# Kernel tuning notes

Hardware: AMD Instinct MI355X
Metric: run time of the kernel (lower is better)

Reference implementation:

```python
import jax, jax.numpy as jnp
import numpy as np


def _gcn(G, A, x, W, b):
    # G: (K,N,N) chebyshev supports, A: (B,N,N) attention, x: (B,N,p)
    s = jnp.einsum('kij,bjp->bkip', G, x)          # graph conv per cheb order
    s = jnp.einsum('bij,bkjp->bikp', A, s)         # attention bmm, -> (B,N,K,p)
    B, N, K, p = s.shape
    s = s.reshape(B, N, K * p)                     # concat over k (k-major blocks)
    return s @ W + b


def setup_inputs() -> dict:
    key = jax.random.key(0)
    ks = jax.random.split(key, 8)
    B, T, N, C = 16, 12, 1024, 1
    K, H = 3, 64
    din = C + H  # 65
    x = jax.random.normal(ks[0], (B, T, N, C), dtype=jnp.float32)
    G = jax.random.normal(ks[1], (K, N, N), dtype=jnp.float32) / np.sqrt(N)
    A = jax.random.uniform(ks[2], (B, N, N), dtype=jnp.float32) / N
    W_gate = jax.random.normal(ks[3], (K * din, 2 * H), dtype=jnp.float32) * 0.02
    b_gate = jnp.zeros((2 * H,), dtype=jnp.float32)
    W_update = jax.random.normal(ks[4], (K * din, H), dtype=jnp.float32) * 0.02
    b_update = jnp.zeros((H,), dtype=jnp.float32)
    W_dec = jax.random.normal(ks[5], (H, 12 * 1), dtype=jnp.float32) * 0.02
    b_dec = jnp.zeros((12,), dtype=jnp.float32)
    return {"x": x, "G": G, "A": A, "W_gate": W_gate, "b_gate": b_gate,
            "W_update": W_update, "b_update": b_update, "W_dec": W_dec, "b_dec": b_dec}


def reference(x, G, A, W_gate, b_gate, W_update, b_update, W_dec, b_dec):
    B, T, N, _ = x.shape
    H = W_update.shape[1]
    out_steps, output_dim = 12, 1

    def step(h, xt):
        combined = jnp.concatenate([xt, h], axis=-1)              # (B,N,din)
        zr = jax.nn.sigmoid(_gcn(G, A, combined, W_gate, b_gate))  # (B,N,2H)
        z, r = zr[..., :H], zr[..., H:]
        cand = jnp.concatenate([xt, r * h], axis=-1)
        hc = jnp.tanh(_gcn(G, A, cand, W_update, b_update))
        h_new = z * hc + (1.0 - z) * h
        return h_new, None

    h0 = jnp.zeros((B, N, H), dtype=x.dtype)
    h_last, _ = jax.lax.scan(step, h0, jnp.swapaxes(x, 0, 1))      # scan over T
    out = h_last @ W_dec + b_dec                                   # (B,N,out_steps*output_dim)
    out = out.reshape(B, N, out_steps, output_dim)
    return jnp.transpose(out, (0, 2, 1, 3))                        # (B,out_steps,N,output_dim)
```

## Files before the change

kernel.cpp:

```cpp
#include <hip/hip_runtime.h>

#define B_  16
#define T_  12
#define N_  1024
#define K_  3
#define H_  64
#define DIN 65
#define KH  192
#define OG  128

typedef _Float16 f16x4 __attribute__((ext_vector_type(4)));
typedef _Float16 f16x8 __attribute__((ext_vector_type(8)));
typedef float    f32x4 __attribute__((ext_vector_type(4)));

static const size_t OFF_H   = 0;
static const size_t OFF_ZB  = 1048576;
static const size_t OFF_S2  = 2097152;
static const size_t OFF_HTA = 2686976;
static const size_t OFF_HTB = 3211264;
static const size_t OFF_S1  = 3735552;
static const size_t OFF_WGT = 4030464;
static const size_t OFF_WUT = 4042752;
static const size_t OFF_WX  = 4048896;
static const size_t OFF_GT  = 4049472;
static const size_t OFF_AG  = 5622336;

__global__ __launch_bounds__(256) void k_repack(const float* __restrict__ Wg,
                                                const float* __restrict__ Wu,
                                                _Float16* __restrict__ wghT,
                                                _Float16* __restrict__ wuhT,
                                                float* __restrict__ wx) {
    const float inv = 1.0f / 1024.0f;
    int idx = blockIdx.x * 256 + threadIdx.x;
    if (idx < 128 * 192) {
        int o = idx / 192, d = idx % 192;
        int k = d / 64, c = d % 64;
        wghT[idx] = (_Float16)(Wg[(size_t)(k * DIN + 1 + c) * OG + o] * inv);
    } else if (idx < 128 * 192 + 64 * 192) {
        int j = idx - 128 * 192;
        int o = j / 192, d = j % 192;
        int k = d / 64, c = d % 64;
        wuhT[j] = (_Float16)(Wu[(size_t)(k * DIN + 1 + c) * H_ + o] * inv);
    } else if (idx < 128 * 192 + 64 * 192 + 576) {
        int j = idx - 128 * 192 - 64 * 192;
        if (j < 384) { int k = j >> 7, o = j & 127; wx[j] = Wg[(size_t)(k * DIN) * OG + o] * inv; }
        else { int j2 = j - 384; int k = j2 >> 6, o = j2 & 63; wx[j] = Wu[(size_t)(k * DIN) * H_ + o] * inv; }
    }
}

__global__ __launch_bounds__(256) void k_gtr(const float* __restrict__ G,
                                             _Float16* __restrict__ GfT) {
    int bx = blockIdx.x;
    int kk = bx >> 8, rem = bx & 255, ti = rem >> 4, tj = rem & 15;
    int i0 = ti * 64, j0 = tj * 64;
    __shared__ _Float16 s[64][72];
    int tid = threadIdx.x;
    int r = tid >> 2, cb = (tid & 3) * 16;
    const float* Gp = G + ((size_t)kk << 20) + ((size_t)(i0 + r) << 10) + j0 + cb;
    #pragma unroll
    for (int q = 0; q < 4; ++q) {
        float4 v = *(const float4*)&Gp[q * 4];
        f16x4 hv = {(_Float16)v.x, (_Float16)v.y, (_Float16)v.z, (_Float16)v.w};
        *(f16x4*)&s[r][cb + q * 4] = hv;
    }
    __syncthreads();
    alignas(16) _Float16 tmp[16];
    #pragma unroll
    for (int q = 0; q < 16; ++q) tmp[q] = s[cb + q][r];
    _Float16* outp = GfT + ((size_t)kk << 20) + ((size_t)(j0 + r) << 10) + i0 + cb;
    *(f16x8*)&outp[0] = *(f16x8*)&tmp[0];
    *(f16x8*)&outp[8] = *(f16x8*)&tmp[8];
}

__global__ __launch_bounds__(256) void k_ag(const float* __restrict__ A,
                                            const _Float16* __restrict__ GfT,
                                            _Float16* __restrict__ AG) {
    int bx = blockIdx.x;
    int inst = bx >> 6, tile = bx & 63;
    int b = inst / 3, kk = inst % 3;
    int i0 = (tile >> 3) * 128, j0 = (tile & 7) * 128;
    __shared__ _Float16 sA[2][128][72], sB[2][128][72];
    int tid = threadIdx.x;
    int w = tid >> 6, lane = tid & 63, ln = lane & 15, kg = lane >> 4;
    int mq = (w & 1) * 64, nq = (w >> 1) * 64;
    int srow = tid >> 1, cb = (tid & 1) * 32;
    const float*    qa = A   + ((size_t)b << 20)  + ((size_t)(i0 + srow) << 10) + cb;
    const _Float16* qb = GfT + ((size_t)kk << 20) + ((size_t)(j0 + srow) << 10) + cb;

    f32x4 acc[4][4];
    #pragma unroll
    for (int mt = 0; mt < 4; ++mt)
        #pragma unroll
        for (int nt = 0; nt < 4; ++nt) acc[mt][nt] = (f32x4){0.f, 0.f, 0.f, 0.f};

    float4 ra[8]; f16x8 rb[4];
    #pragma unroll
    for (int q = 0; q < 8; ++q) ra[q] = *(const float4*)&qa[q * 4];
    #pragma unroll
    for (int q = 0; q < 4; ++q) rb[q] = *(const f16x8*)&qb[q * 8];
    #pragma unroll
    for (int q = 0; q < 4; ++q) {
        float4 u = ra[2*q], v = ra[2*q+1];
        f16x8 hv = {(_Float16)(u.x*1024.f), (_Float16)(u.y*1024.f), (_Float16)(u.z*1024.f), (_Float16)(u.w*1024.f),
                    (_Float16)(v.x*1024.f), (_Float16)(v.y*1024.f), (_Float16)(v.z*1024.f), (_Float16)(v.w*1024.f)};
        *(f16x8*)&sA[0][srow][cb + q * 8] = hv;
        *(f16x8*)&sB[0][srow][cb + q * 8] = rb[q];
    }
    __syncthreads();

    for (int tt = 0; tt < 16; ++tt) {
        int cur = tt & 1;
        if (tt < 15) {
            int kn = (tt + 1) * 64;
            #pragma unroll
            for (int q = 0; q < 8; ++q) ra[q] = *(const float4*)&qa[kn + q * 4];
            #pragma unroll
            for (int q = 0; q < 4; ++q) rb[q] = *(const f16x8*)&qb[kn + q * 8];
        }
        #pragma unroll
        for (int ks = 0; ks < 2; ++ks) {
            int ko = ks * 32 + kg * 8;
            f16x8 a[4], bfr[4];
            #pragma unroll
            for (int mt = 0; mt < 4; ++mt) a[mt] = *(const f16x8*)&sA[cur][mq + mt * 16 + ln][ko];
            #pragma unroll
            for (int nt = 0; nt < 4; ++nt) bfr[nt] = *(const f16x8*)&sB[cur][nq + nt * 16 + ln][ko];
            #pragma unroll
            for (int mt = 0; mt < 4; ++mt)
                #pragma unroll
                for (int nt = 0; nt < 4; ++nt)
                    acc[mt][nt] = __builtin_amdgcn_mfma_f32_16x16x32_f16(a[mt], bfr[nt], acc[mt][nt], 0, 0, 0);
        }
        if (tt < 15) {
            int nb = cur ^ 1;
            #pragma unroll
            for (int q = 0; q < 4; ++q) {
                float4 u = ra[2*q], v = ra[2*q+1];
                f16x8 hv = {(_Float16)(u.x*1024.f), (_Float16)(u.y*1024.f), (_Float16)(u.z*1024.f), (_Float16)(u.w*1024.f),
                            (_Float16)(v.x*1024.f), (_Float16)(v.y*1024.f), (_Float16)(v.z*1024.f), (_Float16)(v.w*1024.f)};
                *(f16x8*)&sA[nb][srow][cb + q * 8] = hv;
                *(f16x8*)&sB[nb][srow][cb + q * 8] = rb[q];
            }
            __syncthreads();
        }
    }

    _Float16* outp = AG + ((size_t)(b * 3 + kk) << 20);
    #pragma unroll
    for (int mt = 0; mt < 4; ++mt)
        #pragma unroll
        for (int r = 0; r < 4; ++r) {
            int i = i0 + mq + mt * 16 + kg * 4 + r;
            #pragma unroll
            for (int nt = 0; nt < 4; ++nt) {
                int j = j0 + nq + nt * 16 + ln;
                outp[((size_t)i << 10) + j] = (_Float16)acc[mt][nt][r];
            }
        }
}

__global__ __launch_bounds__(256) void k_s1b(const float* __restrict__ G,
                                             const float* __restrict__ x,
                                             _Float16* __restrict__ S1) {
    int bx = blockIdx.x;
    int nh = bx & 1, it = (bx >> 1) & 15, kk = bx >> 5;
    int i0 = it * 64, m0 = nh * 96;
    __shared__ _Float16 sA[64][72], sB[96][72];
    int tid = threadIdx.x, wid = tid >> 6, ln = tid & 15, kl = (tid & 63) >> 4;
    const float* Gk = G + (size_t)kk * N_ * N_;
    f32x4 acc[6];
    #pragma unroll
    for (int n = 0; n < 6; ++n) acc[n] = (f32x4){0.f, 0.f, 0.f, 0.f};
    for (int kc = 0; kc < N_; kc += 64) {
        #pragma unroll
        for (int it2 = 0; it2 < 4; ++it2) {
            int idx = it2 * 256 + tid; int row = idx >> 4, c4 = (idx & 15) * 4;
            float4 g = *(const float4*)&Gk[(size_t)(i0 + row) * N_ + kc + c4];
            f16x4 hv = {(_Float16)g.x, (_Float16)g.y, (_Float16)g.z, (_Float16)g.w};
            *(f16x4*)&sA[row][c4] = hv;
        }
        #pragma unroll
        for (int it2 = 0; it2 < 6; ++it2) {
            int idx = it2 * 256 + tid; int row = idx >> 4, c4 = (idx & 15) * 4;
            float4 g = *(const float4*)&x[(size_t)(m0 + row) * N_ + kc + c4];
            f16x4 hv = {(_Float16)g.x, (_Float16)g.y, (_Float16)g.z, (_Float16)g.w};
            *(f16x4*)&sB[row][c4] = hv;
        }
        __syncthreads();
        #pragma unroll
        for (int ks = 0; ks < 4; ++ks) {
            int ko = ks * 16 + kl * 4;
            f16x4 a = *(const f16x4*)&sA[wid * 16 + ln][ko];
            #pragma unroll
            for (int n = 0; n < 6; ++n) {
                f16x4 b = *(const f16x4*)&sB[n * 16 + ln][ko];
                acc[n] = __builtin_amdgcn_mfma_f32_16x16x16f16(a, b, acc[n], 0, 0, 0);
            }
        }
        __syncthreads();
    }
    #pragma unroll
    for (int n = 0; n < 6; ++n) {
        int m = m0 + n * 16 + ln;
        #pragma unroll
        for (int r = 0; r < 4; ++r) {
            int i = i0 + wid * 16 + kl * 4 + r;
            S1[(((size_t)kk * 192 + m) << 10) + i] = (_Float16)acc[n][r];
        }
    }
}

__global__ __launch_bounds__(256) void k_s2b(const float* __restrict__ A,
                                             const _Float16* __restrict__ S1,
                                             float* __restrict__ S2) {
    int bx = blockIdx.x; int it = bx & 15, b = bx >> 4; int i0 = it * 64;
    __shared__ _Float16 sA[64][72], sB[48][72];
    int tid = threadIdx.x, wid = tid >> 6, ln = tid & 15, kl = (tid & 63) >> 4;
    const float* Ab = A + (size_t)b * N_ * N_;
    f32x4 acc[3];
    #pragma unroll
    for (int n = 0; n < 3; ++n) acc[n] = (f32x4){0.f, 0.f, 0.f, 0.f};
    for (int kc = 0; kc < N_; kc += 64) {
        #pragma unroll
        for (int it2 = 0; it2 < 4; ++it2) {
            int idx = it2 * 256 + tid; int row = idx >> 4, c4 = (idx & 15) * 4;
            float4 a4 = *(const float4*)&Ab[(size_t)(i0 + row) * N_ + kc + c4];
            f16x4 hv = {(_Float16)(a4.x * 1024.f), (_Float16)(a4.y * 1024.f),
                        (_Float16)(a4.z * 1024.f), (_Float16)(a4.w * 1024.f)};
            *(f16x4*)&sA[row][c4] = hv;
        }
        for (int idx = tid; idx < 288; idx += 256) {
            int row = idx >> 3, c8 = (idx & 7) * 8;
            int kq = row / 12, tq = row - kq * 12;
            *(uint4*)&sB[row][c8] = *(const uint4*)&S1[(((size_t)kq * 192 + b * T_ + tq) << 10) + kc + c8];
        }
        __syncthreads();
        #pragma unroll
        for (int ks = 0; ks < 4; ++ks) {
            int ko = ks * 16 + kl * 4;
            f16x4 a = *(const f16x4*)&sA[wid * 16 + ln][ko];
            #pragma unroll
            for (int n = 0; n < 3; ++n) {
                f16x4 b = *(const f16x4*)&sB[n * 16 + ln][ko];
                acc[n] = __builtin_amdgcn_mfma_f32_16x16x16f16(a, b, acc[n], 0, 0, 0);
            }
        }
        __syncthreads();
    }
    #pragma unroll
    for (int n = 0; n < 3; ++n) {
        int col = n * 16 + ln;
        if (col < 36) {
            int kq = col / 12, tq = col - kq * 12;
            #pragma unroll
            for (int r = 0; r < 4; ++r) {
                int i = i0 + wid * 16 + kl * 4 + r;
                S2[(((size_t)(b * 3 + kq) * T_ + tq) << 10) + i] = acc[n][r];
            }
        }
    }
}

__global__ __launch_bounds__(256) void k_fzr(const _Float16* __restrict__ AG,
                                             const _Float16* __restrict__ HtIn,
                                             const _Float16* __restrict__ wghT,
                                             const float* __restrict__ wx,
                                             const float* __restrict__ bg,
                                             const float* __restrict__ S2,
                                             const float* __restrict__ h,
                                             float* __restrict__ zb,
                                             _Float16* __restrict__ HtOut, int t) {
    int bx = blockIdx.x; int it = bx & 31, b = bx >> 5; int i0 = it * 32;
    __shared__ __align__(16) char smem[46080];
    _Float16 (*sA)[96][72] = reinterpret_cast<_Float16(*)[96][72]>(smem);
    _Float16 (*sB)[64][72] = reinterpret_cast<_Float16(*)[64][72]>(smem + 27648);
    _Float16 (*sZ)[200]    = reinterpret_cast<_Float16(*)[200]>(smem);
    _Float16 (*sW)[72]     = reinterpret_cast<_Float16(*)[72]>(smem + 12800);
    __shared__ float sS2[3][32];
    __shared__ float sWX[384];
    __shared__ float sBias[128];
    int tid = threadIdx.x;
    int w = tid >> 6, lane = tid & 63, ln = lane & 15, kg = lane >> 4;
    if (tid < 96) { int k = tid >> 5, il = tid & 31; sS2[k][il] = S2[(((size_t)(b * 3 + k) * T_ + t) << 10) + i0 + il]; }
    for (int q = tid; q < 384; q += 256) sWX[q] = wx[q];
    if (tid < 128) sBias[tid] = bg[tid];

    int srow = tid >> 3, sc8 = (tid & 7) * 8;
    const _Float16* pa0 = AG + ((size_t)(b * 3 + 0) << 20) + ((size_t)(i0 + srow) << 10) + sc8;
    const _Float16* pa1 = AG + ((size_t)(b * 3 + 1) << 20) + ((size_t)(i0 + srow) << 10) + sc8;
    const _Float16* pa2 = AG + ((size_t)(b * 3 + 2) << 20) + ((size_t)(i0 + srow) << 10) + sc8;
    const _Float16* pb0 = HtIn + ((size_t)b << 16) + ((size_t)srow << 10) + sc8;
    const _Float16* pb1 = HtIn + ((size_t)b << 16) + ((size_t)(srow + 32) << 10) + sc8;

    f32x4 acc[2][3];
    #pragma unroll
    for (int m = 0; m < 2; ++m)
        #pragma unroll
        for (int n = 0; n < 3; ++n) acc[m][n] = (f32x4){0.f, 0.f, 0.f, 0.f};

    f16x8 rA0 = *(const f16x8*)pa0, rA1 = *(const f16x8*)pa1, rA2 = *(const f16x8*)pa2;
    f16x8 rB0 = *(const f16x8*)pb0, rB1 = *(const f16x8*)pb1;
    *(f16x8*)&sA[0][srow][sc8] = rA0;
    *(f16x8*)&sA[0][32 + srow][sc8] = rA1;
    *(f16x8*)&sA[0][64 + srow][sc8] = rA2;
    *(f16x8*)&sB[0][srow][sc8] = rB0;
    *(f16x8*)&sB[0][srow + 32][sc8] = rB1;
    __syncthreads();

    int kbF = (w * 3) >> 2, kbL = (w * 3 + 2) >> 2;
    for (int tt = 0; tt < 16; ++tt) {
        int cur = tt & 1;
        if (tt < 15) {
            int kn = (tt + 1) * 64;
            rA0 = *(const f16x8*)&pa0[kn]; rA1 = *(const f16x8*)&pa1[kn]; rA2 = *(const f16x8*)&pa2[kn];
            rB0 = *(const f16x8*)&pb0[kn]; rB1 = *(const f16x8*)&pb1[kn];
        }
        #pragma unroll
        for (int ks = 0; ks < 2; ++ks) {
            int ko = ks * 32 + kg * 8;
            f16x8 aF0 = *(const f16x8*)&sA[cur][kbF * 32 + ln][ko];
            f16x8 aF1 = *(const f16x8*)&sA[cur][kbF * 32 + 16 + ln][ko];
            f16x8 aL0 = *(const f16x8*)&sA[cur][kbL * 32 + ln][ko];
            f16x8 aL1 = *(const f16x8*)&sA[cur][kbL * 32 + 16 + ln][ko];
            #pragma unroll
            for (int ni = 0; ni < 3; ++ni) {
                int ct = w * 3 + ni;
                f16x8 bb = *(const f16x8*)&sB[cur][(ct & 3) * 16 + ln][ko];
                bool late = (ct >> 2) != kbF;
                f16x8 a0 = late ? aL0 : aF0;
                f16x8 a1 = late ? aL1 : aF1;
                acc[0][ni] = __builtin_amdgcn_mfma_f32_16x16x32_f16(a0, bb, acc[0][ni], 0, 0, 0);
                acc[1][ni] = __builtin_amdgcn_mfma_f32_16x16x32_f16(a1, bb, acc[1][ni], 0, 0, 0);
            }
        }
        if (tt < 15) {
            int nb = cur ^ 1;
            *(f16x8*)&sA[nb][srow][sc8] = rA0;
            *(f16x8*)&sA[nb][32 + srow][sc8] = rA1;
            *(f16x8*)&sA[nb][64 + srow][sc8] = rA2;
            *(f16x8*)&sB[nb][srow][sc8] = rB0;
            *(f16x8*)&sB[nb][srow + 32][sc8] = rB1;
            __syncthreads();
        }
    }
    __syncthreads();

    #pragma unroll
    for (int m = 0; m < 2; ++m)
        #pragma unroll
        for (int ni = 0; ni < 3; ++ni)
            #pragma unroll
            for (int r = 0; r < 4; ++r)
                sZ[m * 16 + kg * 4 + r][(w * 3 + ni) * 16 + ln] = (_Float16)acc[m][ni][r];

    f32x4 e[2][2];
    #pragma unroll
    for (int m = 0; m < 2; ++m)
        #pragma unroll
        for (int n = 0; n < 2; ++n) e[m][n] = (f32x4){0.f, 0.f, 0.f, 0.f};
    for (int kc = 0; kc < 192; kc += 64) {
        #pragma unroll
        for (int it2 = 0; it2 < 4; ++it2) {
            int idx = it2 * 256 + tid; int row = idx >> 3, c8 = (idx & 7) * 8;
            *(f16x8*)&sW[row][c8] = *(const f16x8*)&wghT[(size_t)row * 192 + kc + c8];
        }
        __syncthreads();
        #pragma unroll
        for (int ks = 0; ks < 4; ++ks) {
            int ko = ks * 16 + kg * 4;
            f16x4 az0 = *(const f16x4*)&sZ[ln][kc + ko];
            f16x4 az1 = *(const f16x4*)&sZ[16 + ln][kc + ko];
            f16x4 bw0 = *(const f16x4*)&sW[w * 32 + ln][ko];
            f16x4 bw1 = *(const f16x4*)&sW[w * 32 + 16 + ln][ko];
            e[0][0] = __builtin_amdgcn_mfma_f32_16x16x16f16(az0, bw0, e[0][0], 0, 0, 0);
            e[0][1] = __builtin_amdgcn_mfma_f32_16x16x16f16(az0, bw1, e[0][1], 0, 0, 0);
            e[1][0] = __builtin_amdgcn_mfma_f32_16x16x16f16(az1, bw0, e[1][0], 0, 0, 0);
            e[1][1] = __builtin_amdgcn_mfma_f32_16x16x16f16(az1, bw1, e[1][1], 0, 0, 0);
        }
        __syncthreads();
    }

    #pragma unroll
    for (int n = 0; n < 2; ++n) {
        int o = w * 32 + n * 16 + ln;
        float w0 = sWX[o], w1 = sWX[128 + o], w2 = sWX[256 + o], bi = sBias[o];
        if (o < H_) {
            #pragma unroll
            for (int m = 0; m < 2; ++m)
                #pragma unroll
                for (int r = 0; r < 4; ++r) {
                    int il = m * 16 + kg * 4 + r;
                    float pre = e[m][n][r] + w0 * sS2[0][il] + w1 * sS2[1][il] + w2 * sS2[2][il] + bi;
                    float v = 1.0f / (1.0f + expf(-pre));
                    zb[((size_t)((b << 10) + i0 + il)) * H_ + o] = v;
                }
        } else {
            int c = o - H_;
            #pragma unroll
            for (int m = 0; m < 2; ++m) {
                alignas(8) _Float16 hb[4];
                #pragma unroll
                for (int r = 0; r < 4; ++r) {
                    int il = m * 16 + kg * 4 + r;
                    float pre = e[m][n][r] + w0 * sS2[0][il] + w1 * sS2[1][il] + w2 * sS2[2][il] + bi;
                    float v = 1.0f / (1.0f + expf(-pre));
                    hb[r] = (_Float16)(v * h[((size_t)((b << 10) + i0 + il)) * H_ + c]);
                }
                *(f16x4*)&HtOut[((size_t)(b * 64 + c) << 10) + i0 + m * 16 + kg * 4] = *(f16x4*)&hb[0];
            }
        }
    }
}

__global__ __launch_bounds__(256) void k_fup(const _Float16* __restrict__ AG,
                                             const _Float16* __restrict__ HtIn,
                                             const _Float16* __restrict__ wuhT,
                                             const float* __restrict__ wx,
                                             const float* __restrict__ bu,
                                             const float* __restrict__ S2,
                                             const float* __restrict__ zb,
                                             float* __restrict__ h,
                                             _Float16* __restrict__ HtOut, int t) {
    int bx = blockIdx.x; int it = bx & 31, b = bx >> 5; int i0 = it * 32;
    __shared__ __align__(16) char smem[46080];
    _Float16 (*sA)[96][72] = reinterpret_cast<_Float16(*)[96][72]>(smem);
    _Float16 (*sB)[64][72] = reinterpret_cast<_Float16(*)[64][72]>(smem + 27648);
    _Float16 (*sZ)[200]    = reinterpret_cast<_Float16(*)[200]>(smem);
    _Float16 (*sW)[72]     = reinterpret_cast<_Float16(*)[72]>(smem + 12800);
    __shared__ float sS2[3][32];
    __shared__ float sWX[192];
    __shared__ float sBias[64];
    int tid = threadIdx.x;
    int w = tid >> 6, lane = tid & 63, ln = lane & 15, kg = lane >> 4;
    if (tid < 96) { int k = tid >> 5, il = tid & 31; sS2[k][il] = S2[(((size_t)(b * 3 + k) * T_ + t) << 10) + i0 + il]; }
    if (tid < 192) sWX[tid] = wx[384 + tid];
    if (tid < 64) sBias[tid] = bu[tid];

    int srow = tid >> 3, sc8 = (tid & 7) * 8;
    const _Float16* pa0 = AG + ((size_t)(b * 3 + 0) << 20) + ((size_t)(i0 + srow) << 10) + sc8;
    const _Float16* pa1 = AG + ((size_t)(b * 3 + 1) << 20) + ((size_t)(i0 + srow) << 10) + sc8;
    const _Float16* pa2 = AG + ((size_t)(b * 3 + 2) << 20) + ((size_t)(i0 + srow) << 10) + sc8;
    const _Float16* pb0 = HtIn + ((size_t)b << 16) + ((size_t)srow << 10) + sc8;
    const _Float16* pb1 = HtIn + ((size_t)b << 16) + ((size_t)(srow + 32) << 10) + sc8;

    f32x4 acc[2][3];
    #pragma unroll
    for (int m = 0; m < 2; ++m)
        #pragma unroll
        for (int n = 0; n < 3; ++n) acc[m][n] = (f32x4){0.f, 0.f, 0.f, 0.f};

    f16x8 rA0 = *(const f16x8*)pa0, rA1 = *(const f16x8*)pa1, rA2 = *(const f16x8*)pa2;
    f16x8 rB0 = *(const f16x8*)pb0, rB1 = *(const f16x8*)pb1;
    *(f16x8*)&sA[0][srow][sc8] = rA0;
    *(f16x8*)&sA[0][32 + srow][sc8] = rA1;
    *(f16x8*)&sA[0][64 + srow][sc8] = rA2;
    *(f16x8*)&sB[0][srow][sc8] = rB0;
    *(f16x8*)&sB[0][srow + 32][sc8] = rB1;
    __syncthreads();

    int kbF = (w * 3) >> 2, kbL = (w * 3 + 2) >> 2;
    for (int tt = 0; tt < 16; ++tt) {
        int cur = tt & 1;
        if (tt < 15) {
            int kn = (tt + 1) * 64;
            rA0 = *(const f16x8*)&pa0[kn]; rA1 = *(const f16x8*)&pa1[kn]; rA2 = *(const f16x8*)&pa2[kn];
            rB0 = *(const f16x8*)&pb0[kn]; rB1 = *(const f16x8*)&pb1[kn];
        }
        #pragma unroll
        for (int ks = 0; ks < 2; ++ks) {
            int ko = ks * 32 + kg * 8;
            f16x8 aF0 = *(const f16x8*)&sA[cur][kbF * 32 + ln][ko];
            f16x8 aF1 = *(const f16x8*)&sA[cur][kbF * 32 + 16 + ln][ko];
            f16x8 aL0 = *(const f16x8*)&sA[cur][kbL * 32 + ln][ko];
            f16x8 aL1 = *(const f16x8*)&sA[cur][kbL * 32 + 16 + ln][ko];
            #pragma unroll
            for (int ni = 0; ni < 3; ++ni) {
                int ct = w * 3 + ni;
                f16x8 bb = *(const f16x8*)&sB[cur][(ct & 3) * 16 + ln][ko];
                bool late = (ct >> 2) != kbF;
                f16x8 a0 = late ? aL0 : aF0;
                f16x8 a1 = late ? aL1 : aF1;
                acc[0][ni] = __builtin_amdgcn_mfma_f32_16x16x32_f16(a0, bb, acc[0][ni], 0, 0, 0);
                acc[1][ni] = __builtin_amdgcn_mfma_f32_16x16x32_f16(a1, bb, acc[1][ni], 0, 0, 0);
            }
        }
        if (tt < 15) {
            int nb = cur ^ 1;
            *(f16x8*)&sA[nb][srow][sc8] = rA0;
            *(f16x8*)&sA[nb][32 + srow][sc8] = rA1;
            *(f16x8*)&sA[nb][64 + srow][sc8] = rA2;
            *(f16x8*)&sB[nb][srow][sc8] = rB0;
            *(f16x8*)&sB[nb][srow + 32][sc8] = rB1;
            __syncthreads();
        }
    }
    __syncthreads();

    #pragma unroll
    for (int m = 0; m < 2; ++m)
        #pragma unroll
        for (int ni = 0; ni < 3; ++ni)
            #pragma unroll
            for (int r = 0; r < 4; ++r)
                sZ[m * 16 + kg * 4 + r][(w * 3 + ni) * 16 + ln] = (_Float16)acc[m][ni][r];

    f32x4 e[2];
    e[0] = (f32x4){0.f, 0.f, 0.f, 0.f};
    e[1] = (f32x4){0.f, 0.f, 0.f, 0.f};
    for (int kc = 0; kc < 192; kc += 64) {
        #pragma unroll
        for (int it2 = 0; it2 < 2; ++it2) {
            int idx = it2 * 256 + tid; int row = idx >> 3, c8 = (idx & 7) * 8;
            *(f16x8*)&sW[row][c8] = *(const f16x8*)&wuhT[(size_t)row * 192 + kc + c8];
        }
        __syncthreads();
        #pragma unroll
        for (int ks = 0; ks < 4; ++ks) {
            int ko = ks * 16 + kg * 4;
            f16x4 az0 = *(const f16x4*)&sZ[ln][kc + ko];
            f16x4 az1 = *(const f16x4*)&sZ[16 + ln][kc + ko];
            f16x4 bw  = *(const f16x4*)&sW[w * 16 + ln][ko];
            e[0] = __builtin_amdgcn_mfma_f32_16x16x16f16(az0, bw, e[0], 0, 0, 0);
            e[1] = __builtin_amdgcn_mfma_f32_16x16x16f16(az1, bw, e[1], 0, 0, 0);
        }
        __syncthreads();
    }

    int o = w * 16 + ln;
    float w0 = sWX[o], w1 = sWX[64 + o], w2 = sWX[128 + o], bi = sBias[o];
    #pragma unroll
    for (int m = 0; m < 2; ++m) {
        alignas(8) _Float16 hb[4];
        #pragma unroll
        for (int r = 0; r < 4; ++r) {
            int il = m * 16 + kg * 4 + r;
            float pre = e[m][r] + w0 * sS2[0][il] + w1 * sS2[1][il] + w2 * sS2[2][il] + bi;
            float hc = tanhf(pre);
            size_t gi = ((size_t)((b << 10) + i0 + il)) * H_ + o;
            float z = zb[gi], hold = h[gi];
            float hn = z * hc + (1.0f - z) * hold;
            h[gi] = hn;
            hb[r] = (_Float16)hn;
        }
        *(f16x4*)&HtOut[((size_t)(b * 64 + o) << 10) + i0 + m * 16 + kg * 4] = *(f16x4*)&hb[0];
    }
}

__global__ __launch_bounds__(256) void k_dec(const float* __restrict__ h,
                                             const float* __restrict__ Wd,
                                             const float* __restrict__ bd,
                                             float* __restrict__ out) {
    int bx = blockIdx.x;
    int b = bx >> 4, it = bx & 15; int i0 = it * 64;
    __shared__ float hs[64][65];
    __shared__ float Wds[64][12];
    __shared__ float bds[12];
    int tid = threadIdx.x;
    for (int idx = tid; idx < 4096; idx += 256) {
        int r = idx >> 6, c = idx & 63;
        hs[r][c] = h[(size_t)(b * N_ + i0 + r) * H_ + c];
    }
    for (int idx = tid; idx < 768; idx += 256)
        Wds[idx / 12][idx % 12] = Wd[idx];
    if (tid < 12) bds[tid] = bd[tid];
    __syncthreads();
    for (int oidx = tid; oidx < 768; oidx += 256) {
        int i = oidx & 63, tt = oidx >> 6;
        float acc = bds[tt];
        #pragma unroll
        for (int c = 0; c < 64; ++c) acc += hs[i][c] * Wds[c][tt];
        out[(size_t)(b * T_ + tt) * N_ + i0 + i] = acc;
    }
}

extern "C" void kernel_launch(void* const* d_in, const int* in_sizes, int n_in,
                              void* d_out, int out_size, void* d_ws, size_t ws_size,
                              hipStream_t stream) {
    const float* x  = (const float*)d_in[0];
    const float* G  = (const float*)d_in[1];
    const float* A  = (const float*)d_in[2];
    const float* Wg = (const float*)d_in[3];
    const float* bg = (const float*)d_in[4];
    const float* Wu = (const float*)d_in[5];
    const float* bu = (const float*)d_in[6];
    const float* Wd = (const float*)d_in[7];
    const float* bd = (const float*)d_in[8];
    float* out = (float*)d_out;
    float* ws  = (float*)d_ws;

    float* h   = ws + OFF_H;
    float* zb  = ws + OFF_ZB;
    float* S2  = ws + OFF_S2;
    float* wxb = ws + OFF_WX;
    _Float16* HtA  = (_Float16*)(ws + OFF_HTA);
    _Float16* HtB  = (_Float16*)(ws + OFF_HTB);
    _Float16* S1   = (_Float16*)(ws + OFF_S1);
    _Float16* wghT = (_Float16*)(ws + OFF_WGT);
    _Float16* wuhT = (_Float16*)(ws + OFF_WUT);
    _Float16* GfT  = (_Float16*)(ws + OFF_GT);
    _Float16* AG   = (_Float16*)(ws + OFF_AG);

    hipMemsetAsync(h, 0, (size_t)B_ * N_ * H_ * sizeof(float), stream);
    hipMemsetAsync((void*)HtA, 0, (size_t)B_ * N_ * H_ * sizeof(_Float16), stream);
    k_repack<<<147, 256, 0, stream>>>(Wg, Wu, wghT, wuhT, wxb);
    k_gtr<<<768, 256, 0, stream>>>(G, GfT);
    k_ag<<<3072, 256, 0, stream>>>(A, GfT, AG);
    k_s1b<<<96, 256, 0, stream>>>(G, x, S1);
    k_s2b<<<256, 256, 0, stream>>>(A, S1, S2);

    for (int t = 0; t < T_; ++t) {
        k_fzr<<<512, 256, 0, stream>>>(AG, HtA, wghT, wxb, bg, S2, h, zb, HtB, t);
        k_fup<<<512, 256, 0, stream>>>(AG, HtB, wuhT, wxb, bu, S2, zb, h, HtA, t);
    }
    k_dec<<<256, 256, 0, stream>>>(h, Wd, bd, out);
}
```

Baseline: 960.7 us.

## Pre-convert A to fp16 once, swizzle AG block order, halve recurrent row tiles

```diff
diff --git a/kernel.cpp b/kernel.cpp
--- a/kernel.cpp
+++ b/kernel.cpp
@@ -24,6 +24,7 @@
 static const size_t OFF_WX  = 4048896;
 static const size_t OFF_GT  = 4049472;
 static const size_t OFF_AG  = 5622336;
+static const size_t OFF_AF  = 30788160;
 
 __global__ __launch_bounds__(256) void k_repack(const float* __restrict__ Wg,
                                                 const float* __restrict__ Wu,
@@ -48,6 +49,16 @@
     }
 }
 
+__global__ __launch_bounds__(256) void k_acvt(const float* __restrict__ A,
+                                              _Float16* __restrict__ Af) {
+    size_t idx = ((size_t)blockIdx.x * 256 + threadIdx.x) * 8;
+    float4 a = *(const float4*)&A[idx];
+    float4 c = *(const float4*)&A[idx + 4];
+    f16x8 v = {(_Float16)(a.x*1024.f), (_Float16)(a.y*1024.f), (_Float16)(a.z*1024.f), (_Float16)(a.w*1024.f),
+               (_Float16)(c.x*1024.f), (_Float16)(c.y*1024.f), (_Float16)(c.z*1024.f), (_Float16)(c.w*1024.f)};
+    *(f16x8*)&Af[idx] = v;
+}
+
 __global__ __launch_bounds__(256) void k_gtr(const float* __restrict__ G,
                                              _Float16* __restrict__ GfT) {
     int bx = blockIdx.x;
@@ -72,10 +83,11 @@
     *(f16x8*)&outp[8] = *(f16x8*)&tmp[8];
 }
 
-__global__ __launch_bounds__(256) void k_ag(const float* __restrict__ A,
+__global__ __launch_bounds__(256) void k_ag(const _Float16* __restrict__ Af,
                                             const _Float16* __restrict__ GfT,
                                             _Float16* __restrict__ AG) {
-    int bx = blockIdx.x;
+    int bxr = blockIdx.x;
+    int bx = (bxr & 7) * 384 + (bxr >> 3);
     int inst = bx >> 6, tile = bx & 63;
     int b = inst / 3, kk = inst % 3;
     int i0 = (tile >> 3) * 128, j0 = (tile & 7) * 128;
@@ -84,7 +96,7 @@
     int w = tid >> 6, lane = tid & 63, ln = lane & 15, kg = lane >> 4;
     int mq = (w & 1) * 64, nq = (w >> 1) * 64;
     int srow = tid >> 1, cb = (tid & 1) * 32;
-    const float*    qa = A   + ((size_t)b << 20)  + ((size_t)(i0 + srow) << 10) + cb;
+    const _Float16* qa = Af  + ((size_t)b << 20)  + ((size_t)(i0 + srow) << 10) + cb;
     const _Float16* qb = GfT + ((size_t)kk << 20) + ((size_t)(j0 + srow) << 10) + cb;
 
     f32x4 acc[4][4];
@@ -93,17 +105,12 @@
         #pragma unroll
         for (int nt = 0; nt < 4; ++nt) acc[mt][nt] = (f32x4){0.f, 0.f, 0.f, 0.f};
 
-    float4 ra[8]; f16x8 rb[4];
-    #pragma unroll
-    for (int q = 0; q < 8; ++q) ra[q] = *(const float4*)&qa[q * 4];
-    #pragma unroll
-    for (int q = 0; q < 4; ++q) rb[q] = *(const f16x8*)&qb[q * 8];
+    f16x8 ra[4], rb[4];
+    #pragma unroll
+    for (int q = 0; q < 4; ++q) { ra[q] = *(const f16x8*)&qa[q * 8]; rb[q] = *(const f16x8*)&qb[q * 8]; }
     #pragma unroll
     for (int q = 0; q < 4; ++q) {
-        float4 u = ra[2*q], v = ra[2*q+1];
-        f16x8 hv = {(_Float16)(u.x*1024.f), (_Float16)(u.y*1024.f), (_Float16)(u.z*1024.f), (_Float16)(u.w*1024.f),
-                    (_Float16)(v.x*1024.f), (_Float16)(v.y*1024.f), (_Float16)(v.z*1024.f), (_Float16)(v.w*1024.f)};
-        *(f16x8*)&sA[0][srow][cb + q * 8] = hv;
+        *(f16x8*)&sA[0][srow][cb + q * 8] = ra[q];
         *(f16x8*)&sB[0][srow][cb + q * 8] = rb[q];
     }
     __syncthreads();
@@ -113,9 +120,7 @@
         if (tt < 15) {
             int kn = (tt + 1) * 64;
             #pragma unroll
-            for (int q = 0; q < 8; ++q) ra[q] = *(const float4*)&qa[kn + q * 4];
-            #pragma unroll
-            for (int q = 0; q < 4; ++q) rb[q] = *(const f16x8*)&qb[kn + q * 8];
+            for (int q = 0; q < 4; ++q) { ra[q] = *(const f16x8*)&qa[kn + q * 8]; rb[q] = *(const f16x8*)&qb[kn + q * 8]; }
         }
         #pragma unroll
         for (int ks = 0; ks < 2; ++ks) {
@@ -135,10 +140,7 @@
             int nb = cur ^ 1;
             #pragma unroll
             for (int q = 0; q < 4; ++q) {
-                float4 u = ra[2*q], v = ra[2*q+1];
-                f16x8 hv = {(_Float16)(u.x*1024.f), (_Float16)(u.y*1024.f), (_Float16)(u.z*1024.f), (_Float16)(u.w*1024.f),
-                            (_Float16)(v.x*1024.f), (_Float16)(v.y*1024.f), (_Float16)(v.z*1024.f), (_Float16)(v.w*1024.f)};
-                *(f16x8*)&sA[nb][srow][cb + q * 8] = hv;
+                *(f16x8*)&sA[nb][srow][cb + q * 8] = ra[q];
                 *(f16x8*)&sB[nb][srow][cb + q * 8] = rb[q];
             }
             __syncthreads();
@@ -210,24 +212,20 @@
     }
 }
 
-__global__ __launch_bounds__(256) void k_s2b(const float* __restrict__ A,
+__global__ __launch_bounds__(256) void k_s2b(const _Float16* __restrict__ Af,
                                              const _Float16* __restrict__ S1,
                                              float* __restrict__ S2) {
     int bx = blockIdx.x; int it = bx & 15, b = bx >> 4; int i0 = it * 64;
     __shared__ _Float16 sA[64][72], sB[48][72];
     int tid = threadIdx.x, wid = tid >> 6, ln = tid & 15, kl = (tid & 63) >> 4;
-    const float* Ab = A + (size_t)b * N_ * N_;
     f32x4 acc[3];
     #pragma unroll
     for (int n = 0; n < 3; ++n) acc[n] = (f32x4){0.f, 0.f, 0.f, 0.f};
     for (int kc = 0; kc < N_; kc += 64) {
         #pragma unroll
-        for (int it2 = 0; it2 < 4; ++it2) {
-            int idx = it2 * 256 + tid; int row = idx >> 4, c4 = (idx & 15) * 4;
-            float4 a4 = *(const float4*)&Ab[(size_t)(i0 + row) * N_ + kc + c4];
-            f16x4 hv = {(_Float16)(a4.x * 1024.f), (_Float16)(a4.y * 1024.f),
-                        (_Float16)(a4.z * 1024.f), (_Float16)(a4.w * 1024.f)};
-            *(f16x4*)&sA[row][c4] = hv;
+        for (int it2 = 0; it2 < 2; ++it2) {
+            int idx = it2 * 256 + tid; int row = idx >> 3, c8 = (idx & 7) * 8;
+            *(uint4*)&sA[row][c8] = *(const uint4*)&Af[((size_t)b << 20) + ((size_t)(i0 + row) << 10) + kc + c8];
         }
         for (int idx = tid; idx < 288; idx += 256) {
             int row = idx >> 3, c8 = (idx & 7) * 8;
@@ -270,41 +268,48 @@
                                              const float* __restrict__ h,
                                              float* __restrict__ zb,
                                              _Float16* __restrict__ HtOut, int t) {
-    int bx = blockIdx.x; int it = bx & 31, b = bx >> 5; int i0 = it * 32;
-    __shared__ __align__(16) char smem[46080];
-    _Float16 (*sA)[96][72] = reinterpret_cast<_Float16(*)[96][72]>(smem);
-    _Float16 (*sB)[64][72] = reinterpret_cast<_Float16(*)[64][72]>(smem + 27648);
+    int bx = blockIdx.x; int it = bx & 63, b = bx >> 6; int i0 = it * 16;
+    __shared__ __align__(16) char smem[32256];
+    _Float16 (*sA)[48][72] = reinterpret_cast<_Float16(*)[48][72]>(smem);
+    _Float16 (*sB)[64][72] = reinterpret_cast<_Float16(*)[64][72]>(smem + 13824);
     _Float16 (*sZ)[200]    = reinterpret_cast<_Float16(*)[200]>(smem);
-    _Float16 (*sW)[72]     = reinterpret_cast<_Float16(*)[72]>(smem + 12800);
-    __shared__ float sS2[3][32];
+    _Float16 (*sW)[72]     = reinterpret_cast<_Float16(*)[72]>(smem + 6400);
+    __shared__ float sS2[3][16];
     __shared__ float sWX[384];
     __shared__ float sBias[128];
     int tid = threadIdx.x;
     int w = tid >> 6, lane = tid & 63, ln = lane & 15, kg = lane >> 4;
-    if (tid < 96) { int k = tid >> 5, il = tid & 31; sS2[k][il] = S2[(((size_t)(b * 3 + k) * T_ + t) << 10) + i0 + il]; }
+    if (tid < 48) { int k = tid >> 4, il = tid & 15; sS2[k][il] = S2[(((size_t)(b * 3 + k) * T_ + t) << 10) + i0 + il]; }
     for (int q = tid; q < 384; q += 256) sWX[q] = wx[q];
     if (tid < 128) sBias[tid] = bg[tid];
 
-    int srow = tid >> 3, sc8 = (tid & 7) * 8;
-    const _Float16* pa0 = AG + ((size_t)(b * 3 + 0) << 20) + ((size_t)(i0 + srow) << 10) + sc8;
-    const _Float16* pa1 = AG + ((size_t)(b * 3 + 1) << 20) + ((size_t)(i0 + srow) << 10) + sc8;
-    const _Float16* pa2 = AG + ((size_t)(b * 3 + 2) << 20) + ((size_t)(i0 + srow) << 10) + sc8;
-    const _Float16* pb0 = HtIn + ((size_t)b << 16) + ((size_t)srow << 10) + sc8;
-    const _Float16* pb1 = HtIn + ((size_t)b << 16) + ((size_t)(srow + 32) << 10) + sc8;
-
-    f32x4 acc[2][3];
-    #pragma unroll
-    for (int m = 0; m < 2; ++m)
-        #pragma unroll
-        for (int n = 0; n < 3; ++n) acc[m][n] = (f32x4){0.f, 0.f, 0.f, 0.f};
-
-    f16x8 rA0 = *(const f16x8*)pa0, rA1 = *(const f16x8*)pa1, rA2 = *(const f16x8*)pa2;
-    f16x8 rB0 = *(const f16x8*)pb0, rB1 = *(const f16x8*)pb1;
-    *(f16x8*)&sA[0][srow][sc8] = rA0;
-    *(f16x8*)&sA[0][32 + srow][sc8] = rA1;
-    *(f16x8*)&sA[0][64 + srow][sc8] = rA2;
-    *(f16x8*)&sB[0][srow][sc8] = rB0;
-    *(f16x8*)&sB[0][srow + 32][sc8] = rB1;
+    const _Float16* pA[3]; int c4A[3], rowA[3];
+    #pragma unroll
+    for (int q = 0; q < 3; ++q) {
+        int idx = q * 256 + tid; rowA[q] = idx >> 4; c4A[q] = (idx & 15) * 4;
+        int kb = rowA[q] >> 4, rloc = rowA[q] & 15;
+        pA[q] = AG + ((size_t)(b * 3 + kb) << 20) + ((size_t)(i0 + rloc) << 10) + c4A[q];
+    }
+    const _Float16* pB[2]; int c8B[2], rowB[2];
+    #pragma unroll
+    for (int q = 0; q < 2; ++q) {
+        int idx = q * 256 + tid; rowB[q] = idx >> 3; c8B[q] = (idx & 7) * 8;
+        pB[q] = HtIn + ((size_t)b << 16) + ((size_t)rowB[q] << 10) + c8B[q];
+    }
+
+    f32x4 acc[3];
+    #pragma unroll
+    for (int n = 0; n < 3; ++n) acc[n] = (f32x4){0.f, 0.f, 0.f, 0.f};
+
+    f16x4 ra[3]; f16x8 rb[2];
+    #pragma unroll
+    for (int q = 0; q < 3; ++q) ra[q] = *(const f16x4*)pA[q];
+    #pragma unroll
+    for (int q = 0; q < 2; ++q) rb[q] = *(const f16x8*)pB[q];
+    #pragma unroll
+    for (int q = 0; q < 3; ++q) *(f16x4*)&sA[0][rowA[q]][c4A[q]] = ra[q];
+    #pragma unroll
+    for (int q = 0; q < 2; ++q) *(f16x8*)&sB[0][rowB[q]][c8B[q]] = rb[q];
     __syncthreads();
 
     int kbF = (w * 3) >> 2, kbL = (w * 3 + 2) >> 2;
@@ -312,52 +317,44 @@
         int cur = tt & 1;
         if (tt < 15) {
             int kn = (tt + 1) * 64;
-            rA0 = *(const f16x8*)&pa0[kn]; rA1 = *(const f16x8*)&pa1[kn]; rA2 = *(const f16x8*)&pa2[kn];
-            rB0 = *(const f16x8*)&pb0[kn]; rB1 = *(const f16x8*)&pb1[kn];
+            #pragma unroll
+            for (int q = 0; q < 3; ++q) ra[q] = *(const f16x4*)&pA[q][kn];
+            #pragma unroll
+            for (int q = 0; q < 2; ++q) rb[q] = *(const f16x8*)&pB[q][kn];
         }
         #pragma unroll
         for (int ks = 0; ks < 2; ++ks) {
             int ko = ks * 32 + kg * 8;
-            f16x8 aF0 = *(const f16x8*)&sA[cur][kbF * 32 + ln][ko];
-            f16x8 aF1 = *(const f16x8*)&sA[cur][kbF * 32 + 16 + ln][ko];
-            f16x8 aL0 = *(const f16x8*)&sA[cur][kbL * 32 + ln][ko];
-            f16x8 aL1 = *(const f16x8*)&sA[cur][kbL * 32 + 16 + ln][ko];
+            f16x8 aF = *(const f16x8*)&sA[cur][kbF * 16 + ln][ko];
+            f16x8 aL = *(const f16x8*)&sA[cur][kbL * 16 + ln][ko];
             #pragma unroll
             for (int ni = 0; ni < 3; ++ni) {
                 int ct = w * 3 + ni;
                 f16x8 bb = *(const f16x8*)&sB[cur][(ct & 3) * 16 + ln][ko];
-                bool late = (ct >> 2) != kbF;
-                f16x8 a0 = late ? aL0 : aF0;
-                f16x8 a1 = late ? aL1 : aF1;
-                acc[0][ni] = __builtin_amdgcn_mfma_f32_16x16x32_f16(a0, bb, acc[0][ni], 0, 0, 0);
-                acc[1][ni] = __builtin_amdgcn_mfma_f32_16x16x32_f16(a1, bb, acc[1][ni], 0, 0, 0);
+                f16x8 a = ((ct >> 2) != kbF) ? aL : aF;
+                acc[ni] = __builtin_amdgcn_mfma_f32_16x16x32_f16(a, bb, acc[ni], 0, 0, 0);
             }
         }
         if (tt < 15) {
             int nb = cur ^ 1;
-            *(f16x8*)&sA[nb][srow][sc8] = rA0;
-            *(f16x8*)&sA[nb][32 + srow][sc8] = rA1;
-            *(f16x8*)&sA[nb][64 + srow][sc8] = rA2;
-            *(f16x8*)&sB[nb][srow][sc8] = rB0;
-            *(f16x8*)&sB[nb][srow + 32][sc8] = rB1;
+            #pragma unroll
+            for (int q = 0; q < 3; ++q) *(f16x4*)&sA[nb][rowA[q]][c4A[q]] = ra[q];
+            #pragma unroll
+            for (int q = 0; q < 2; ++q) *(f16x8*)&sB[nb][rowB[q]][c8B[q]] = rb[q];
             __syncthreads();
         }
     }
     __syncthreads();
 
     #pragma unroll
-    for (int m = 0; m < 2; ++m)
-        #pragma unroll
-        for (int ni = 0; ni < 3; ++ni)
-            #pragma unroll
-            for (int r = 0; r < 4; ++r)
-                sZ[m * 16 + kg * 4 + r][(w * 3 + ni) * 16 + ln] = (_Float16)acc[m][ni][r];
-
-    f32x4 e[2][2];
-    #pragma unroll
-    for (int m = 0; m < 2; ++m)
-        #pragma unroll
-        for (int n = 0; n < 2; ++n) e[m][n] = (f32x4){0.f, 0.f, 0.f, 0.f};
+    for (int ni = 0; ni < 3; ++ni)
+        #pragma unroll
+        for (int r = 0; r < 4; ++r)
+            sZ[kg * 4 + r][(w * 3 + ni) * 16 + ln] = (_Float16)acc[ni][r];
+
+    f32x4 e[2];
+    e[0] = (f32x4){0.f, 0.f, 0.f, 0.f};
+    e[1] = (f32x4){0.f, 0.f, 0.f, 0.f};
     for (int kc = 0; kc < 192; kc += 64) {
         #pragma unroll
         for (int it2 = 0; it2 < 4; ++it2) {
@@ -368,14 +365,11 @@
         #pragma unroll
         for (int ks = 0; ks < 4; ++ks) {
             int ko = ks * 16 + kg * 4;
-            f16x4 az0 = *(const f16x4*)&sZ[ln][kc + ko];
-            f16x4 az1 = *(const f16x4*)&sZ[16 + ln][kc + ko];
+            f16x4 az  = *(const f16x4*)&sZ[ln][kc + ko];
             f16x4 bw0 = *(const f16x4*)&sW[w * 32 + ln][ko];
             f16x4 bw1 = *(const f16x4*)&sW[w * 32 + 16 + ln][ko];
-            e[0][0] = __builtin_amdgcn_mfma_f32_16x16x16f16(az0, bw0, e[0][0], 0, 0, 0);
-            e[0][1] = __builtin_amdgcn_mfma_f32_16x16x16f16(az0, bw1, e[0][1], 0, 0, 0);
-            e[1][0] = __builtin_amdgcn_mfma_f32_16x16x16f16(az1, bw0, e[1][0], 0, 0, 0);
-            e[1][1] = __builtin_amdgcn_mfma_f32_16x16x16f16(az1, bw1, e[1][1], 0, 0, 0);
+            e[0] = __builtin_amdgcn_mfma_f32_16x16x16f16(az, bw0, e[0], 0, 0, 0);
+            e[1] = __builtin_amdgcn_mfma_f32_16x16x16f16(az, bw1, e[1], 0, 0, 0);
         }
         __syncthreads();
     }
@@ -386,28 +380,23 @@
         float w0 = sWX[o], w1 = sWX[128 + o], w2 = sWX[256 + o], bi = sBias[o];
         if (o < H_) {
             #pragma unroll
-            for (int m = 0; m < 2; ++m)
-                #pragma unroll
-                for (int r = 0; r < 4; ++r) {
-                    int il = m * 16 + kg * 4 + r;
-                    float pre = e[m][n][r] + w0 * sS2[0][il] + w1 * sS2[1][il] + w2 * sS2[2][il] + bi;
-                    float v = 1.0f / (1.0f + expf(-pre));
-                    zb[((size_t)((b << 10) + i0 + il)) * H_ + o] = v;
-                }
+            for (int r = 0; r < 4; ++r) {
+                int il = kg * 4 + r;
+                float pre = e[n][r] + w0 * sS2[0][il] + w1 * sS2[1][il] + w2 * sS2[2][il] + bi;
+                float v = 1.0f / (1.0f + expf(-pre));
+                zb[((size_t)((b << 10) + i0 + il)) * H_ + o] = v;
+            }
         } else {
             int c = o - H_;
-            #pragma unroll
-            for (int m = 0; m < 2; ++m) {
-                alignas(8) _Float16 hb[4];
-                #pragma unroll
-                for (int r = 0; r < 4; ++r) {
-                    int il = m * 16 + kg * 4 + r;
-                    float pre = e[m][n][r] + w0 * sS2[0][il] + w1 * sS2[1][il] + w2 * sS2[2][il] + bi;
-                    float v = 1.0f / (1.0f + expf(-pre));
-                    hb[r] = (_Float16)(v * h[((size_t)((b << 10) + i0 + il)) * H_ + c]);
-                }
-                *(f16x4*)&HtOut[((size_t)(b * 64 + c) << 10) + i0 + m * 16 + kg * 4] = *(f16x4*)&hb[0];
-            }
+            alignas(8) _Float16 hb[4];
+            #pragma unroll
+            for (int r = 0; r < 4; ++r) {
+                int il = kg * 4 + r;
+                float pre = e[n][r] + w0 * sS2[0][il] + w1 * sS2[1][il] + w2 * sS2[2][il] + bi;
+                float v = 1.0f / (1.0f + expf(-pre));
+                hb[r] = (_Float16)(v * h[((size_t)((b << 10) + i0 + il)) * H_ + c]);
+            }
+            *(f16x4*)&HtOut[((size_t)(b * 64 + c) << 10) + i0 + kg * 4] = *(f16x4*)&hb[0];
         }
     }
 }
@@ -421,41 +410,48 @@
                                              const float* __restrict__ zb,
                                              float* __restrict__ h,
                                              _Float16* __restrict__ HtOut, int t) {
-    int bx = blockIdx.x; int it = bx & 31, b = bx >> 5; int i0 = it * 32;
-    __shared__ __align__(16) char smem[46080];
-    _Float16 (*sA)[96][72] = reinterpret_cast<_Float16(*)[96][72]>(smem);
-    _Float16 (*sB)[64][72] = reinterpret_cast<_Float16(*)[64][72]>(smem + 27648);
+    int bx = blockIdx.x; int it = bx & 63, b = bx >> 6; int i0 = it * 16;
+    __shared__ __align__(16) char smem[32256];
+    _Float16 (*sA)[48][72] = reinterpret_cast<_Float16(*)[48][72]>(smem);
+    _Float16 (*sB)[64][72] = reinterpret_cast<_Float16(*)[64][72]>(smem + 13824);
     _Float16 (*sZ)[200]    = reinterpret_cast<_Float16(*)[200]>(smem);
-    _Float16 (*sW)[72]     = reinterpret_cast<_Float16(*)[72]>(smem + 12800);
-    __shared__ float sS2[3][32];
+    _Float16 (*sW)[72]     = reinterpret_cast<_Float16(*)[72]>(smem + 6400);
+    __shared__ float sS2[3][16];
     __shared__ float sWX[192];
     __shared__ float sBias[64];
     int tid = threadIdx.x;
     int w = tid >> 6, lane = tid & 63, ln = lane & 15, kg = lane >> 4;
-    if (tid < 96) { int k = tid >> 5, il = tid & 31; sS2[k][il] = S2[(((size_t)(b * 3 + k) * T_ + t) << 10) + i0 + il]; }
+    if (tid < 48) { int k = tid >> 4, il = tid & 15; sS2[k][il] = S2[(((size_t)(b * 3 + k) * T_ + t) << 10) + i0 + il]; }
     if (tid < 192) sWX[tid] = wx[384 + tid];
     if (tid < 64) sBias[tid] = bu[tid];
 
-    int srow = tid >> 3, sc8 = (tid & 7) * 8;
-    const _Float16* pa0 = AG + ((size_t)(b * 3 + 0) << 20) + ((size_t)(i0 + srow) << 10) + sc8;
-    const _Float16* pa1 = AG + ((size_t)(b * 3 + 1) << 20) + ((size_t)(i0 + srow) << 10) + sc8;
-    const _Float16* pa2 = AG + ((size_t)(b * 3 + 2) << 20) + ((size_t)(i0 + srow) << 10) + sc8;
-    const _Float16* pb0 = HtIn + ((size_t)b << 16) + ((size_t)srow << 10) + sc8;
-    const _Float16* pb1 = HtIn + ((size_t)b << 16) + ((size_t)(srow + 32) << 10) + sc8;
-
-    f32x4 acc[2][3];
-    #pragma unroll
-    for (int m = 0; m < 2; ++m)
-        #pragma unroll
-        for (int n = 0; n < 3; ++n) acc[m][n] = (f32x4){0.f, 0.f, 0.f, 0.f};
-
-    f16x8 rA0 = *(const f16x8*)pa0, rA1 = *(const f16x8*)pa1, rA2 = *(const f16x8*)pa2;
-    f16x8 rB0 = *(const f16x8*)pb0, rB1 = *(const f16x8*)pb1;
-    *(f16x8*)&sA[0][srow][sc8] = rA0;
-    *(f16x8*)&sA[0][32 + srow][sc8] = rA1;
-    *(f16x8*)&sA[0][64 + srow][sc8] = rA2;
-    *(f16x8*)&sB[0][srow][sc8] = rB0;
-    *(f16x8*)&sB[0][srow + 32][sc8] = rB1;
+    const _Float16* pA[3]; int c4A[3], rowA[3];
+    #pragma unroll
+    for (int q = 0; q < 3; ++q) {
+        int idx = q * 256 + tid; rowA[q] = idx >> 4; c4A[q] = (idx & 15) * 4;
+        int kb = rowA[q] >> 4, rloc = rowA[q] & 15;
+        pA[q] = AG + ((size_t)(b * 3 + kb) << 20) + ((size_t)(i0 + rloc) << 10) + c4A[q];
+    }
+    const _Float16* pB[2]; int c8B[2], rowB[2];
+    #pragma unroll
+    for (int q = 0; q < 2; ++q) {
+        int idx = q * 256 + tid; rowB[q] = idx >> 3; c8B[q] = (idx & 7) * 8;
+        pB[q] = HtIn + ((size_t)b << 16) + ((size_t)rowB[q] << 10) + c8B[q];
+    }
+
+    f32x4 acc[3];
+    #pragma unroll
+    for (int n = 0; n < 3; ++n) acc[n] = (f32x4){0.f, 0.f, 0.f, 0.f};
+
+    f16x4 ra[3]; f16x8 rb[2];
+    #pragma unroll
+    for (int q = 0; q < 3; ++q) ra[q] = *(const f16x4*)pA[q];
+    #pragma unroll
+    for (int q = 0; q < 2; ++q) rb[q] = *(const f16x8*)pB[q];
+    #pragma unroll
+    for (int q = 0; q < 3; ++q) *(f16x4*)&sA[0][rowA[q]][c4A[q]] = ra[q];
+    #pragma unroll
+    for (int q = 0; q < 2; ++q) *(f16x8*)&sB[0][rowB[q]][c8B[q]] = rb[q];
     __syncthreads();
 
     int kbF = (w * 3) >> 2, kbL = (w * 3 + 2) >> 2;
@@ -463,50 +459,42 @@
         int cur = tt & 1;
         if (tt < 15) {
             int kn = (tt + 1) * 64;
-            rA0 = *(const f16x8*)&pa0[kn]; rA1 = *(const f16x8*)&pa1[kn]; rA2 = *(const f16x8*)&pa2[kn];
-            rB0 = *(const f16x8*)&pb0[kn]; rB1 = *(const f16x8*)&pb1[kn];
+            #pragma unroll
+            for (int q = 0; q < 3; ++q) ra[q] = *(const f16x4*)&pA[q][kn];
+            #pragma unroll
+            for (int q = 0; q < 2; ++q) rb[q] = *(const f16x8*)&pB[q][kn];
         }
         #pragma unroll
         for (int ks = 0; ks < 2; ++ks) {
             int ko = ks * 32 + kg * 8;
-            f16x8 aF0 = *(const f16x8*)&sA[cur][kbF * 32 + ln][ko];
-            f16x8 aF1 = *(const f16x8*)&sA[cur][kbF * 32 + 16 + ln][ko];
-            f16x8 aL0 = *(const f16x8*)&sA[cur][kbL * 32 + ln][ko];
-            f16x8 aL1 = *(const f16x8*)&sA[cur][kbL * 32 + 16 + ln][ko];
+            f16x8 aF = *(const f16x8*)&sA[cur][kbF * 16 + ln][ko];
+            f16x8 aL = *(const f16x8*)&sA[cur][kbL * 16 + ln][ko];
             #pragma unroll
             for (int ni = 0; ni < 3; ++ni) {
                 int ct = w * 3 + ni;
                 f16x8 bb = *(const f16x8*)&sB[cur][(ct & 3) * 16 + ln][ko];
-                bool late = (ct >> 2) != kbF;
-                f16x8 a0 = late ? aL0 : aF0;
-                f16x8 a1 = late ? aL1 : aF1;
-                acc[0][ni] = __builtin_amdgcn_mfma_f32_16x16x32_f16(a0, bb, acc[0][ni], 0, 0, 0);
-                acc[1][ni] = __builtin_amdgcn_mfma_f32_16x16x32_f16(a1, bb, acc[1][ni], 0, 0, 0);
+                f16x8 a = ((ct >> 2) != kbF) ? aL : aF;
+                acc[ni] = __builtin_amdgcn_mfma_f32_16x16x32_f16(a, bb, acc[ni], 0, 0, 0);
             }
         }
         if (tt < 15) {
             int nb = cur ^ 1;
-            *(f16x8*)&sA[nb][srow][sc8] = rA0;
-            *(f16x8*)&sA[nb][32 + srow][sc8] = rA1;
-            *(f16x8*)&sA[nb][64 + srow][sc8] = rA2;
-            *(f16x8*)&sB[nb][srow][sc8] = rB0;
-            *(f16x8*)&sB[nb][srow + 32][sc8] = rB1;
+            #pragma unroll
+            for (int q = 0; q < 3; ++q) *(f16x4*)&sA[nb][rowA[q]][c4A[q]] = ra[q];
+            #pragma unroll
+            for (int q = 0; q < 2; ++q) *(f16x8*)&sB[nb][rowB[q]][c8B[q]] = rb[q];
             __syncthreads();
         }
     }
     __syncthreads();
 
     #pragma unroll
-    for (int m = 0; m < 2; ++m)
-        #pragma unroll
-        for (int ni = 0; ni < 3; ++ni)
-            #pragma unroll
-            for (int r = 0; r < 4; ++r)
-                sZ[m * 16 + kg * 4 + r][(w * 3 + ni) * 16 + ln] = (_Float16)acc[m][ni][r];
-
-    f32x4 e[2];
-    e[0] = (f32x4){0.f, 0.f, 0.f, 0.f};
-    e[1] = (f32x4){0.f, 0.f, 0.f, 0.f};
+    for (int ni = 0; ni < 3; ++ni)
+        #pragma unroll
+        for (int r = 0; r < 4; ++r)
+            sZ[kg * 4 + r][(w * 3 + ni) * 16 + ln] = (_Float16)acc[ni][r];
+
+    f32x4 e = (f32x4){0.f, 0.f, 0.f, 0.f};
     for (int kc = 0; kc < 192; kc += 64) {
         #pragma unroll
         for (int it2 = 0; it2 < 2; ++it2) {
@@ -517,33 +505,28 @@
         #pragma unroll
         for (int ks = 0; ks < 4; ++ks) {
             int ko = ks * 16 + kg * 4;
-            f16x4 az0 = *(const f16x4*)&sZ[ln][kc + ko];
-            f16x4 az1 = *(const f16x4*)&sZ[16 + ln][kc + ko];
-            f16x4 bw  = *(const f16x4*)&sW[w * 16 + ln][ko];
-            e[0] = __builtin_amdgcn_mfma_f32_16x16x16f16(az0, bw, e[0], 0, 0, 0);
-            e[1] = __builtin_amdgcn_mfma_f32_16x16x16f16(az1, bw, e[1], 0, 0, 0);
+            f16x4 az = *(const f16x4*)&sZ[ln][kc + ko];
+            f16x4 bw = *(const f16x4*)&sW[w * 16 + ln][ko];
+            e = __builtin_amdgcn_mfma_f32_16x16x16f16(az, bw, e, 0, 0, 0);
         }
         __syncthreads();
     }
 
     int o = w * 16 + ln;
     float w0 = sWX[o], w1 = sWX[64 + o], w2 = sWX[128 + o], bi = sBias[o];
-    #pragma unroll
-    for (int m = 0; m < 2; ++m) {
-        alignas(8) _Float16 hb[4];
-        #pragma unroll
-        for (int r = 0; r < 4; ++r) {
-            int il = m * 16 + kg * 4 + r;
-            float pre = e[m][r] + w0 * sS2[0][il] + w1 * sS2[1][il] + w2 * sS2[2][il] + bi;
-            float hc = tanhf(pre);
-            size_t gi = ((size_t)((b << 10) + i0 + il)) * H_ + o;
-            float z = zb[gi], hold = h[gi];
-            float hn = z * hc + (1.0f - z) * hold;
-            h[gi] = hn;
-            hb[r] = (_Float16)hn;
-        }
-        *(f16x4*)&HtOut[((size_t)(b * 64 + o) << 10) + i0 + m * 16 + kg * 4] = *(f16x4*)&hb[0];
-    }
+    alignas(8) _Float16 hb[4];
+    #pragma unroll
+    for (int r = 0; r < 4; ++r) {
+        int il = kg * 4 + r;
+        float pre = e[r] + w0 * sS2[0][il] + w1 * sS2[1][il] + w2 * sS2[2][il] + bi;
+        float hc = tanhf(pre);
+        size_t gi = ((size_t)((b << 10) + i0 + il)) * H_ + o;
+        float z = zb[gi], hold = h[gi];
+        float hn = z * hc + (1.0f - z) * hold;
+        h[gi] = hn;
+        hb[r] = (_Float16)hn;
+    }
+    *(f16x4*)&HtOut[((size_t)(b * 64 + o) << 10) + i0 + kg * 4] = *(f16x4*)&hb[0];
 }
 
 __global__ __launch_bounds__(256) void k_dec(const float* __restrict__ h,
@@ -599,18 +582,20 @@
     _Float16* wuhT = (_Float16*)(ws + OFF_WUT);
     _Float16* GfT  = (_Float16*)(ws + OFF_GT);
     _Float16* AG   = (_Float16*)(ws + OFF_AG);
+    _Float16* Af   = (_Float16*)(ws + OFF_AF);
 
     hipMemsetAsync(h, 0, (size_t)B_ * N_ * H_ * sizeof(float), stream);
     hipMemsetAsync((void*)HtA, 0, (size_t)B_ * N_ * H_ * sizeof(_Float16), stream);
     k_repack<<<147, 256, 0, stream>>>(Wg, Wu, wghT, wuhT, wxb);
     k_gtr<<<768, 256, 0, stream>>>(G, GfT);
-    k_ag<<<3072, 256, 0, stream>>>(A, GfT, AG);
+    k_acvt<<<8192, 256, 0, stream>>>(A, Af);
+    k_ag<<<3072, 256, 0, stream>>>(Af, GfT, AG);
     k_s1b<<<96, 256, 0, stream>>>(G, x, S1);
-    k_s2b<<<256, 256, 0, stream>>>(A, S1, S2);
+    k_s2b<<<256, 256, 0, stream>>>(Af, S1, S2);
 
     for (int t = 0; t < T_; ++t) {
-        k_fzr<<<512, 256, 0, stream>>>(AG, HtA, wghT, wxb, bg, S2, h, zb, HtB, t);
-        k_fup<<<512, 256, 0, stream>>>(AG, HtB, wuhT, wxb, bu, S2, zb, h, HtA, t);
+        k_fzr<<<1024, 256, 0, stream>>>(AG, HtA, wghT, wxb, bg, S2, h, zb, HtB, t);
+        k_fup<<<1024, 256, 0, stream>>>(AG, HtB, wuhT, wxb, bu, S2, zb, h, HtA, t);
     }
     k_dec<<<256, 256, 0, stream>>>(h, Wd, bd, out);
 }
```

After: 823.3 us. 1.17x faster.
